# Kernel tuning notes

Measured on AMD Instinct MI355X. Metric: run time of the kernel, lower is better.

## Reference

```python
import jax, jax.numpy as jnp
import numpy as np


def setup_inputs() -> dict:
    key = jax.random.key(0)
    k1, k2, k3 = jax.random.split(key, 3)
    B, S, H, R, I = 4, 2048, 4096, 8, 11008
    return {
        "x": jax.random.normal(k1, (B, S, H), dtype=jnp.float32),
        "w1": jax.random.normal(k2, (2, H, R), dtype=jnp.float32),
        "w2": jax.random.normal(k3, (2, R, I), dtype=jnp.float32),
        "sparsity_pct": 50,  # sparsity = 0.50
    }


def reference(x, w1, w2, sparsity_pct):
    sparsity = sparsity_pct / 100.0
    H = x.shape[-1]
    I = w2.shape[-1]
    # flatten tokens: [N, H]; both branches share the same input (expand(2, ...))
    xt = x.reshape(-1, H)
    # low-rank projections per branch: [2, N, R] -> [2, N, I]
    p = jnp.einsum('nh,ghr->gnr', xt, w1)
    q = jnp.einsum('gnr,gri->gni', p, w2)
    # fused SiLU-gate: silu(branch0) * branch1 -> [N, I]
    g = jax.nn.silu(q[0]) * q[1]
    # L2 norm across tokens (dim=0) -> [I]
    n = jnp.sqrt(jnp.sum(g * g, axis=0))
    # top-k channel selection over intermediate_size
    k = int(I * (1.0 - sparsity))
    _, idx = jax.lax.top_k(n, k)
    return idx.reshape(-1)
```

## Files before the change

### kernel.cpp

```cpp
#include <hip/hip_runtime.h>
#include <stdint.h>

#define NTOK 8192
#define HDIM 4096
#define NI   11008

__global__ void k0_cvt(const float* __restrict__ w1, double* __restrict__ w1d) {
    int i = blockIdx.x * 256 + threadIdx.x;
    if (i < 2 * HDIM * 8) w1d[i] = (double)w1[i];
}

__global__ __launch_bounds__(512) void k1a_proj(const float* __restrict__ x,
                                                const double* __restrict__ w1d,
                                                double* __restrict__ p4) {
    __shared__ double lds[4][64][16];
    const int tid = threadIdx.x;
    const int wv = __builtin_amdgcn_readfirstlane(tid >> 6);
    const int lane = tid & 63;
    const int hb = blockIdx.x >> 7;
    const int tg = blockIdx.x & 127;
    const int token = tg * 64 + lane;
    const int hbase = hb * 512 + wv * 64;

    const float4* xr = (const float4*)(x + (size_t)token * HDIM + hbase);
    const double* wb0 = w1d + (size_t)hbase * 8;
    const double* wb1 = w1d + 32768 + (size_t)hbase * 8;

    double acc[16];
#pragma unroll
    for (int j = 0; j < 16; ++j) acc[j] = 0.0;

#pragma unroll 1
    for (int it = 0; it < 4; ++it) {
        float4 a0 = xr[it * 4 + 0];
        float4 a1 = xr[it * 4 + 1];
        float4 a2 = xr[it * 4 + 2];
        float4 a3 = xr[it * 4 + 3];
        const double* w0  = wb0 + (size_t)it * 128;
        const double* w1p = wb1 + (size_t)it * 128;
        float xs[16] = {a0.x, a0.y, a0.z, a0.w, a1.x, a1.y, a1.z, a1.w,
                        a2.x, a2.y, a2.z, a2.w, a3.x, a3.y, a3.z, a3.w};
#pragma unroll
        for (int m = 0; m < 16; ++m) {
            double xd = (double)xs[m];
#pragma unroll
            for (int r = 0; r < 8; ++r) {
                acc[r]     = __fma_rn(xd, w0[m * 8 + r],  acc[r]);
                acc[8 + r] = __fma_rn(xd, w1p[m * 8 + r], acc[8 + r]);
            }
        }
    }
    if (wv < 4) {
#pragma unroll
        for (int j = 0; j < 16; ++j) lds[wv][lane][j] = acc[j];
    }
    __syncthreads();
    if (wv >= 4) {
#pragma unroll
        for (int j = 0; j < 16; ++j) lds[wv - 4][lane][j] += acc[j];
    }
    __syncthreads();
#pragma unroll
    for (int s = 0; s < 2; ++s) {
        int slot = tid + s * 512;
        int t = slot >> 4, j = slot & 15;
        double v = 0.0;
#pragma unroll
        for (int k = 0; k < 4; ++k) v += lds[k][t][j];
        p4[(size_t)hb * (NTOK * 16) + ((size_t)tg * 64 + t) * 16 + j] = v;
    }
}

__global__ void k1b_comb(const double* __restrict__ p4, float* __restrict__ p) {
    int i = blockIdx.x * 256 + threadIdx.x;
    double v = 0.0;
#pragma unroll
    for (int hb = 0; hb < 8; ++hb)
        v += p4[(size_t)hb * (NTOK * 16) + i];
    p[i] = (float)v;
}

__device__ __forceinline__ double g2_tok32(const float* __restrict__ pr,
                                           const float* waf, const float* wbf) {
    float q0 = 0.0f, q1 = 0.0f;
#pragma unroll
    for (int r = 0; r < 8; ++r) {
        q0 = __builtin_fmaf(pr[r],     waf[r], q0);
        q1 = __builtin_fmaf(pr[8 + r], wbf[r], q1);
    }
    float y = q0 * -1.44269504088896340736f;
    float ef;
    asm("v_exp_f32 %0, %1" : "=v"(ef) : "v"(y));
    float d = 1.0f + ef;
    float s = __builtin_amdgcn_rcpf(d);
    float g = (q0 * s) * q1;
    double gd = (double)g;
    return gd * gd;
}

__global__ __launch_bounds__(512, 4) void k2_nsq(const float* __restrict__ p,
                                                 const float* __restrict__ w2,
                                                 double* __restrict__ nsq_part) {
    __shared__ float  lds_p[256][20];
    __shared__ double lds_s[4][128];
    const int ib  = blockIdx.x % 86;
    const int c   = blockIdx.x / 86;
    const int ch  = threadIdx.x & 127;
    const int sub = threadIdx.x >> 7;
    const int i   = ib * 128 + ch;

    float waf[8], wbf[8];
#pragma unroll
    for (int r = 0; r < 8; ++r) {
        waf[r] = w2[(size_t)r * NI + i];
        wbf[r] = w2[(size_t)(8 + r) * NI + i];
    }
    double acc0 = 0.0, acc1 = 0.0;
    const int row = threadIdx.x >> 1;
    const int hf  = threadIdx.x & 1;
#pragma unroll 1
    for (int pass = 0; pass < 2; ++pass) {
        __syncthreads();
        {
            const float4* src = (const float4*)(p +
                ((size_t)c * 512 + pass * 256 + row) * 16 + hf * 8);
            float4 v0 = src[0], v1 = src[1];
            float4* dst = (float4*)&lds_p[row][hf * 8];
            dst[0] = v0;
            dst[1] = v1;
        }
        __syncthreads();
        const int t0 = sub * 64;
        for (int tl = t0; tl < t0 + 64; tl += 2) {
            acc0 = __fma_rn(1.0, g2_tok32(lds_p[tl],     waf, wbf), acc0);
            acc1 = __fma_rn(1.0, g2_tok32(lds_p[tl + 1], waf, wbf), acc1);
        }
    }
    __syncthreads();
    lds_s[sub][ch] = acc0 + acc1;
    __syncthreads();
    if (threadIdx.x < 128) {
        double s = 0.0;
#pragma unroll
        for (int q = 0; q < 4; ++q) s += lds_s[q][ch];
        nsq_part[(size_t)c * NI + i] = s;
    }
}

__device__ inline double dither_xi(unsigned int i, unsigned long long seed) {
    unsigned long long z = (unsigned long long)i * 0x9E3779B97F4A7C15ULL + seed;
    z = (z ^ (z >> 30)) * 0xBF58476D1CE4E5B9ULL;
    z = (z ^ (z >> 27)) * 0x94D049BB133111EBULL;
    z ^= z >> 31;
    return 2.0 * ((double)(z >> 11) * (1.0 / 9007199254740992.0)) - 1.0;
}

__global__ void k2b_key(const double* __restrict__ nsq_part,
                        unsigned long long* __restrict__ keys,
                        unsigned int* __restrict__ rank) {
    const int i = blockIdx.x * 256 + threadIdx.x;
    double s = 0.0, comp = 0.0;
#pragma unroll
    for (int c = 0; c < 16; ++c) {
        double yk = nsq_part[(size_t)c * NI + i] - comp;
        double tk = s + yk;
        comp = (tk - s) - yk;
        s = tk;
    }
    s = s * (1.0 + 2e-8 * dither_xi((unsigned int)i, 0x9E2025C0FFEE5EEDULL));
    float nf = (float)sqrt(s);
    unsigned int fb = __float_as_uint(nf);
    keys[i] = ((unsigned long long)fb << 32) |
              (unsigned long long)(0x0FFFFFFFu - (unsigned int)i);
    rank[i] = 0u;
}

__global__ __launch_bounds__(256) void k3_rank(const unsigned long long* __restrict__ keys,
                                               unsigned int* __restrict__ rank) {
    const int ib = blockIdx.x % 43;
    const int jc = blockIdx.x / 43;
    const int i  = ib * 256 + threadIdx.x;
    const unsigned long long ki = keys[i];
    unsigned int cnt = 0;
    const int j0 = jc * (NI / 32);
#pragma unroll 8
    for (int j = j0; j < j0 + NI / 32; ++j)
        cnt += (keys[j] > ki) ? 1u : 0u;
    if (cnt) atomicAdd(&rank[i], cnt);
}

__global__ void k4_scatter(const unsigned int* __restrict__ rank,
                           int* __restrict__ out, int k) {
    const int i = blockIdx.x * 256 + threadIdx.x;
    const unsigned int r = rank[i];
    if (r < (unsigned int)k) out[r] = (int)i;
}

extern "C" void kernel_launch(void* const* d_in, const int* in_sizes, int n_in,
                              void* d_out, int out_size, void* d_ws, size_t ws_size,
                              hipStream_t stream) {
    const float* x  = (const float*)d_in[0];
    const float* w1 = (const float*)d_in[1];
    const float* w2 = (const float*)d_in[2];
    char* ws = (char*)d_ws;
    double*             w1d  = (double*)(ws + 0);
    float*              pbuf = (float*)(ws + 524288);
    double*             nsq  = (double*)(ws + 1572864);
    unsigned long long* keys = (unsigned long long*)(ws + 2981888);
    unsigned int*       rank = (unsigned int*)(ws + 3069952);
    double*             p4   = (double*)(ws + 4194304);
    int* out = (int*)d_out;

    hipLaunchKernelGGL(k0_cvt,     dim3(256),     dim3(256), 0, stream, w1, w1d);
    hipLaunchKernelGGL(k1a_proj,   dim3(1024),    dim3(512), 0, stream, x, w1d, p4);
    hipLaunchKernelGGL(k1b_comb,   dim3(512),     dim3(256), 0, stream, p4, pbuf);
    hipLaunchKernelGGL(k2_nsq,     dim3(86 * 16), dim3(512), 0, stream, pbuf, w2, nsq);
    hipLaunchKernelGGL(k2b_key,    dim3(43),      dim3(256), 0, stream, nsq, keys, rank);
    hipLaunchKernelGGL(k3_rank,    dim3(43 * 32), dim3(256), 0, stream, keys, rank);
    hipLaunchKernelGGL(k4_scatter, dim3(43),      dim3(256), 0, stream, rank, out, out_size);
}
```

Measured before the change: 151.0 us.

## Stage x tiles through LDS with coalesced loads in projection kernel

The projection kernel now loads 64x128 tiles of x cooperatively through shared memory with row-contiguous float4 loads, where before each lane read its own token's row with stride. Each block covers 1024 hidden dims over 8 chunks instead of 512, which halves the grid and the number of partial sums the combine kernel must add. The aim is better global-load coalescing for the x stream, which dominates memory traffic. The cost is extra barriers per chunk, LDS round trips, and fewer blocks in flight.

```diff
diff --git a/kernel.cpp b/kernel.cpp
--- a/kernel.cpp
+++ b/kernel.cpp
@@ -13,51 +13,60 @@
 __global__ __launch_bounds__(512) void k1a_proj(const float* __restrict__ x,
                                                 const double* __restrict__ w1d,
                                                 double* __restrict__ p4) {
-    __shared__ double lds[4][64][16];
+    __shared__ union {
+        float  xt[64][129];
+        double ac[4][64][17];
+    } sm;
     const int tid = threadIdx.x;
     const int wv = __builtin_amdgcn_readfirstlane(tid >> 6);
     const int lane = tid & 63;
-    const int hb = blockIdx.x >> 7;
+    const int hq = blockIdx.x >> 7;
     const int tg = blockIdx.x & 127;
-    const int token = tg * 64 + lane;
-    const int hbase = hb * 512 + wv * 64;
-
-    const float4* xr = (const float4*)(x + (size_t)token * HDIM + hbase);
-    const double* wb0 = w1d + (size_t)hbase * 8;
-    const double* wb1 = w1d + 32768 + (size_t)hbase * 8;
+    const int tok0 = tg * 64;
 
     double acc[16];
 #pragma unroll
     for (int j = 0; j < 16; ++j) acc[j] = 0.0;
 
+    const int srow = tid >> 5;
+    const int scol = tid & 31;
+
 #pragma unroll 1
-    for (int it = 0; it < 4; ++it) {
-        float4 a0 = xr[it * 4 + 0];
-        float4 a1 = xr[it * 4 + 1];
-        float4 a2 = xr[it * 4 + 2];
-        float4 a3 = xr[it * 4 + 3];
-        const double* w0  = wb0 + (size_t)it * 128;
-        const double* w1p = wb1 + (size_t)it * 128;
-        float xs[16] = {a0.x, a0.y, a0.z, a0.w, a1.x, a1.y, a1.z, a1.w,
-                        a2.x, a2.y, a2.z, a2.w, a3.x, a3.y, a3.z, a3.w};
-#pragma unroll
-        for (int m = 0; m < 16; ++m) {
-            double xd = (double)xs[m];
+    for (int c = 0; c < 8; ++c) {
+        const int hbase = hq * 1024 + c * 128;
+        __syncthreads();
+#pragma unroll
+        for (int k = 0; k < 4; ++k) {
+            int r = srow + k * 16;
+            float4 v = *(const float4*)(x + (size_t)(tok0 + r) * HDIM
+                                          + hbase + scol * 4);
+            sm.xt[r][scol * 4 + 0] = v.x;
+            sm.xt[r][scol * 4 + 1] = v.y;
+            sm.xt[r][scol * 4 + 2] = v.z;
+            sm.xt[r][scol * 4 + 3] = v.w;
+        }
+        __syncthreads();
+        const double* wb0 = w1d + (size_t)(hbase + wv * 16) * 8;
+        const double* wb1 = w1d + 32768 + (size_t)(hbase + wv * 16) * 8;
+#pragma unroll
+        for (int k = 0; k < 16; ++k) {
+            double xd = (double)sm.xt[lane][wv * 16 + k];
 #pragma unroll
             for (int r = 0; r < 8; ++r) {
-                acc[r]     = __fma_rn(xd, w0[m * 8 + r],  acc[r]);
-                acc[8 + r] = __fma_rn(xd, w1p[m * 8 + r], acc[8 + r]);
+                acc[r]     = __fma_rn(xd, wb0[k * 8 + r], acc[r]);
+                acc[8 + r] = __fma_rn(xd, wb1[k * 8 + r], acc[8 + r]);
             }
         }
     }
+    __syncthreads();
     if (wv < 4) {
 #pragma unroll
-        for (int j = 0; j < 16; ++j) lds[wv][lane][j] = acc[j];
+        for (int j = 0; j < 16; ++j) sm.ac[wv][lane][j] = acc[j];
     }
     __syncthreads();
     if (wv >= 4) {
 #pragma unroll
-        for (int j = 0; j < 16; ++j) lds[wv - 4][lane][j] += acc[j];
+        for (int j = 0; j < 16; ++j) sm.ac[wv - 4][lane][j] += acc[j];
     }
     __syncthreads();
 #pragma unroll
@@ -66,8 +75,8 @@
         int t = slot >> 4, j = slot & 15;
         double v = 0.0;
 #pragma unroll
-        for (int k = 0; k < 4; ++k) v += lds[k][t][j];
-        p4[(size_t)hb * (NTOK * 16) + ((size_t)tg * 64 + t) * 16 + j] = v;
+        for (int k = 0; k < 4; ++k) v += sm.ac[k][t][j];
+        p4[(size_t)hq * (NTOK * 16) + ((size_t)(tok0 + t)) * 16 + j] = v;
     }
 }
 
@@ -75,8 +84,8 @@
     int i = blockIdx.x * 256 + threadIdx.x;
     double v = 0.0;
 #pragma unroll
-    for (int hb = 0; hb < 8; ++hb)
-        v += p4[(size_t)hb * (NTOK * 16) + i];
+    for (int hq = 0; hq < 4; ++hq)
+        v += p4[(size_t)hq * (NTOK * 16) + i];
     p[i] = (float)v;
 }
 
@@ -212,7 +221,7 @@
     int* out = (int*)d_out;
 
     hipLaunchKernelGGL(k0_cvt,     dim3(256),     dim3(256), 0, stream, w1, w1d);
-    hipLaunchKernelGGL(k1a_proj,   dim3(1024),    dim3(512), 0, stream, x, w1d, p4);
+    hipLaunchKernelGGL(k1a_proj,   dim3(512),     dim3(512), 0, stream, x, w1d, p4);
     hipLaunchKernelGGL(k1b_comb,   dim3(512),     dim3(256), 0, stream, p4, pbuf);
     hipLaunchKernelGGL(k2_nsq,     dim3(86 * 16), dim3(512), 0, stream, pbuf, w2, nsq);
     hipLaunchKernelGGL(k2b_key,    dim3(43),      dim3(256), 0, stream, nsq, keys, rank);
```

Result: faster. 129.6 us (median of 3 runs) (-14.2%).
